# Kernel tuning notes

Measured on AMD Instinct MI355X. Metric: run time of the kernel, lower is better.

The kernel has to match this reference:

```python
import jax, jax.numpy as jnp
import numpy as np
from jax import lax

B, S, IN, H, C = 128, 128, 512, 256, 256  # batch, num_sentences, word_hidden*2, sentence_hidden, context
BN_EPS = 1e-5


def setup_inputs() -> dict:
    key = jax.random.key(0)
    ks = jax.random.split(key, 16)
    u = lambda k, shape: jax.random.uniform(k, shape, minval=-0.1, maxval=0.1, dtype=jnp.float32)
    return {
        "x": jax.random.normal(ks[0], (B, S, IN), jnp.float32),
        "sent_hidden_stat": jnp.zeros((2, B, H), jnp.float32),  # unused by forward (as in original)
        "num_sentences_lens": jax.random.randint(ks[1], (B,), 1, S + 1),
        # bidirectional GRU weights (PyTorch layout: [3H, in], gate order r,z,n)
        "w_ih_f": u(ks[2], (3 * H, IN)), "w_hh_f": u(ks[3], (3 * H, H)),
        "b_ih_f": u(ks[4], (3 * H,)),   "b_hh_f": u(ks[5], (3 * H,)),
        "w_ih_b": u(ks[6], (3 * H, IN)), "w_hh_b": u(ks[7], (3 * H, H)),
        "b_ih_b": u(ks[8], (3 * H,)),   "b_hh_b": u(ks[9], (3 * H,)),
        # sentence projection Linear(2H -> C)
        "proj_w": u(ks[10], (C, 2 * H)), "proj_b": u(ks[11], (C,)),
        # BatchNorm1d(num_features=S) affine params
        "bn_gamma": jnp.ones((S,), jnp.float32), "bn_beta": jnp.zeros((S,), jnp.float32),
        # sentence context vector [C, 1]
        "context": u(ks[12], (C, 1)),
    }


def _gru_dir(x, w_ih, w_hh, b_ih, b_hh):
    """Single-direction GRU over x: [B, T, IN] -> [B, T, H] (PyTorch GRU math)."""
    Hd = w_hh.shape[1]
    xp = jnp.einsum('bti,gi->tbg', x, w_ih) + b_ih  # [T, B, 3H], input projections precomputed

    def step(h, xpt):
        hp = h @ w_hh.T + b_hh
        xr, xz, xn = jnp.split(xpt, 3, axis=-1)
        hr, hz, hn = jnp.split(hp, 3, axis=-1)
        r = jax.nn.sigmoid(xr + hr)
        z = jax.nn.sigmoid(xz + hz)
        n = jnp.tanh(xn + r * hn)
        h_new = (1.0 - z) * n + z * h
        return h_new, h_new

    h0 = jnp.zeros((x.shape[0], Hd), x.dtype)
    _, ys = lax.scan(step, h0, xp)
    return jnp.swapaxes(ys, 0, 1)  # [B, T, H]


def reference(x, sent_hidden_stat, num_sentences_lens,
              w_ih_f, w_hh_f, b_ih_f, b_hh_f,
              w_ih_b, w_hh_b, b_ih_b, b_hh_b,
              proj_w, proj_b, bn_gamma, bn_beta, context):
    # Bidirectional GRU over sentences
    out_f = _gru_dir(x, w_ih_f, w_hh_f, b_ih_f, b_hh_f)
    out_b = _gru_dir(x[:, ::-1], w_ih_b, w_hh_b, b_ih_b, b_hh_b)[:, ::-1]
    out = jnp.concatenate([out_f, out_b], axis=-1)  # [B, S, 2H]

    # _fetch/get_mask: zero out positions beyond each document's sentence count
    mask = (jnp.arange(out.shape[1])[None, :] < num_sentences_lens[:, None]).astype(out.dtype)
    out = out * mask[:, :, None]

    # projection -> BatchNorm1d(num_features=S, training stats) -> ReLU
    proj = jnp.einsum('bsd,cd->bsc', out, proj_w) + proj_b  # [B, S, C]
    mu = proj.mean(axis=(0, 2), keepdims=True)
    var = jnp.mean((proj - mu) ** 2, axis=(0, 2), keepdims=True)
    bn = (proj - mu) / jnp.sqrt(var + BN_EPS) * bn_gamma[None, :, None] + bn_beta[None, :, None]
    p = jax.nn.relu(bn)

    # additive attention pooling over sentences
    scores = jnp.einsum('bsc,co->bs', p, context)  # [B, S]
    attn = jax.nn.softmax(scores, axis=1)
    return jnp.einsum('bs,bsd->bd', attn, out)  # [B, 2H]
```

## Files before the change

### kernel.cpp

```cpp
#include <hip/hip_runtime.h>
#include <hip/hip_bf16.h>

#define B_   128
#define S_   128
#define IN_  512
#define H_   256
#define G3_  768
#define C_   256
#define D2H_ 512

typedef short bf16x8 __attribute__((ext_vector_type(8)));
typedef float f32x4  __attribute__((ext_vector_type(4)));

static __device__ __forceinline__ short f2bf(float f) {
  unsigned u = __float_as_uint(f);
  return (short)((u + 0x7fffu + ((u >> 16) & 1u)) >> 16);
}
static __device__ __forceinline__ float bf2f(unsigned short v) {
  return __uint_as_float((unsigned)v << 16);
}

static __device__ __forceinline__ void async16(const void* g, const void* l) {
  __builtin_amdgcn_global_load_lds(
      (const __attribute__((address_space(1))) void*)g,
      (__attribute__((address_space(3))) void*)l, 16, 0, 0);
}

__global__ __launch_bounds__(1024) void pack_wh(
    const float* __restrict__ whf, const float* __restrict__ whb,
    unsigned short* __restrict__ wp)
{
  const int o = blockIdx.x * 1024 + threadIdx.x;
  const int j    = o & 7;
  const int lane = (o >> 3) & 63;
  const int kk   = (o >> 9) & 7;
  const int tt   = (o >> 12) & 1;
  const int rest = o >> 13;
  const int g    = rest % 3;
  const int wv   = (rest / 3) & 7;
  const int dir  = rest / 24;
  const float* w = dir ? whb : whf;
  const int row = wv * 32 + tt * 16 + (lane & 15);
  const int k   = kk * 32 + (lane >> 4) * 8 + j;
  wp[o] = (unsigned short)f2bf(w[(size_t)(g * H_ + row) * H_ + k]);
}

__global__ __launch_bounds__(256) void xp_gemm_bf(
    const float* __restrict__ x,
    const float* __restrict__ wf, const float* __restrict__ wb,
    const float* __restrict__ bif, const float* __restrict__ bhf,
    const float* __restrict__ bib, const float* __restrict__ bhb,
    unsigned short* __restrict__ xpf, unsigned short* __restrict__ xpb)
{
  const int sb = blockIdx.x;
  const int bn = blockIdx.y;
  const bool fwd = (bn < 6);
  const float* __restrict__ wsrc = fwd ? wf : wb;
  const float* __restrict__ bi   = fwd ? bif : bib;
  const float* __restrict__ bh   = fwd ? bhf : bhb;
  const int nloc0 = (fwd ? bn : bn - 6) * 128;

  __shared__ __align__(16) unsigned short As[128][56];
  __shared__ __align__(16) unsigned short Bs[128][56];

  const int tid  = threadIdx.x;
  const int wave = tid >> 6, lane = tid & 63;
  const int col  = lane & 15, lg = lane >> 4;
  const int wm   = wave >> 1, wn = wave & 1;
  const int rr   = tid >> 1;
  const int hf   = (tid & 1) * 16;

  const float* ax = x    + ((size_t)(rr * 128 + sb) * IN_ + hf);
  const float* bx = wsrc + ((size_t)(nloc0 + rr) * IN_ + hf);

  f32x4 acc[4][4];
#pragma unroll
  for (int i = 0; i < 4; ++i)
#pragma unroll
    for (int j = 0; j < 4; ++j) acc[i][j] = f32x4{0.f, 0.f, 0.f, 0.f};

  for (int k0 = 0; k0 < IN_; k0 += 32) {
    float4 a0 = *(const float4*)(ax + k0);
    float4 a1 = *(const float4*)(ax + k0 + 4);
    float4 a2 = *(const float4*)(ax + k0 + 8);
    float4 a3 = *(const float4*)(ax + k0 + 12);
    float4 c0 = *(const float4*)(bx + k0);
    float4 c1 = *(const float4*)(bx + k0 + 4);
    float4 c2 = *(const float4*)(bx + k0 + 8);
    float4 c3 = *(const float4*)(bx + k0 + 12);
    __syncthreads();
    {
      bf16x8 p0, p1;
      p0[0]=f2bf(a0.x); p0[1]=f2bf(a0.y); p0[2]=f2bf(a0.z); p0[3]=f2bf(a0.w);
      p0[4]=f2bf(a1.x); p0[5]=f2bf(a1.y); p0[6]=f2bf(a1.z); p0[7]=f2bf(a1.w);
      p1[0]=f2bf(a2.x); p1[1]=f2bf(a2.y); p1[2]=f2bf(a2.z); p1[3]=f2bf(a2.w);
      p1[4]=f2bf(a3.x); p1[5]=f2bf(a3.y); p1[6]=f2bf(a3.z); p1[7]=f2bf(a3.w);
      *(bf16x8*)&As[rr][hf]     = p0;
      *(bf16x8*)&As[rr][hf + 8] = p1;
      p0[0]=f2bf(c0.x); p0[1]=f2bf(c0.y); p0[2]=f2bf(c0.z); p0[3]=f2bf(c0.w);
      p0[4]=f2bf(c1.x); p0[5]=f2bf(c1.y); p0[6]=f2bf(c1.z); p0[7]=f2bf(c1.w);
      p1[0]=f2bf(c2.x); p1[1]=f2bf(c2.y); p1[2]=f2bf(c2.z); p1[3]=f2bf(c2.w);
      p1[4]=f2bf(c3.x); p1[5]=f2bf(c3.y); p1[6]=f2bf(c3.z); p1[7]=f2bf(c3.w);
      *(bf16x8*)&Bs[rr][hf]     = p0;
      *(bf16x8*)&Bs[rr][hf + 8] = p1;
    }
    __syncthreads();
    bf16x8 af[4], bfv[4];
#pragma unroll
    for (int mi = 0; mi < 4; ++mi)
      af[mi] = *(const bf16x8*)&As[wm * 64 + mi * 16 + col][lg * 8];
#pragma unroll
    for (int ni = 0; ni < 4; ++ni)
      bfv[ni] = *(const bf16x8*)&Bs[wn * 64 + ni * 16 + col][lg * 8];
#pragma unroll
    for (int mi = 0; mi < 4; ++mi)
#pragma unroll
      for (int ni = 0; ni < 4; ++ni)
        acc[mi][ni] = __builtin_amdgcn_mfma_f32_16x16x32_bf16(af[mi], bfv[ni], acc[mi][ni], 0, 0, 0);
  }

  const int t = fwd ? sb : (S_ - 1 - sb);
  unsigned short* __restrict__ dstbase = fwd ? xpf : xpb;
#pragma unroll
  for (int ni = 0; ni < 4; ++ni) {
    const int g = nloc0 + wn * 64 + ni * 16 + col;
    const float bias = bi[g] + (g < 2 * H_ ? bh[g] : 0.f);
#pragma unroll
    for (int mi = 0; mi < 4; ++mi) {
      const int grp = wm * 16 + mi * 4 + lg;
      ushort4 o;
      o.x = (unsigned short)f2bf(acc[mi][ni][0] + bias);
      o.y = (unsigned short)f2bf(acc[mi][ni][1] + bias);
      o.z = (unsigned short)f2bf(acc[mi][ni][2] + bias);
      o.w = (unsigned short)f2bf(acc[mi][ni][3] + bias);
      *(ushort4*)(dstbase + (((size_t)t * 32 + grp) * G3_ + g) * 4) = o;
    }
  }
}

__global__ __launch_bounds__(512, 2) void gru_mfma(
    const unsigned short* __restrict__ xpf, const unsigned short* __restrict__ xpb,
    const unsigned short* __restrict__ wp,
    const float* __restrict__ bhf, const float* __restrict__ bhb,
    const int* __restrict__ lens, float* __restrict__ out)
{
  const int dir  = blockIdx.x >> 5;
  const int grpb = blockIdx.x & 31;
  const int b0   = grpb * 4;
  const unsigned short* __restrict__ xp = dir ? xpb : xpf;
  const float* __restrict__ bhh = dir ? bhb : bhf;

  const int tid  = threadIdx.x;
  const int wave = tid >> 6;
  const int lane = tid & 63;
  const int col  = lane & 15;
  const int lg   = lane >> 4;
  const int gb0  = wave * 32 + col;

  __shared__ __align__(16) unsigned short hlds[2][32][16][8];
  __shared__ __align__(16) unsigned short xlds[2][G3_ * 4];

  ((int4*)hlds)[tid]       = int4{0, 0, 0, 0};
  ((int4*)hlds)[512 + tid] = int4{0, 0, 0, 0};

  {
    const unsigned short* base = xp + (size_t)grpb * (G3_ * 4);
    if (tid < 384)
      async16(base + (size_t)tid * 8, (const char*)&xlds[0][0] + wave * 1024);
  }

  const unsigned short* wpb = wp + (size_t)(dir * 8 + wave) * 24576 + lane * 8;

  bf16x8 wrz[2][2][8];
#pragma unroll
  for (int tt = 0; tt < 2; ++tt)
#pragma unroll
    for (int g = 0; g < 2; ++g)
#pragma unroll
      for (int kk = 0; kk < 8; ++kk)
        wrz[tt][g][kk] = *(const bf16x8*)(wpb + (((g * 2 + tt) * 8 + kk) << 9));

  float bhn[2];
  bhn[0] = bhh[2 * H_ + gb0];
  bhn[1] = bhh[2 * H_ + gb0 + 16];

  int len_[4];
#pragma unroll
  for (int i = 0; i < 4; ++i) len_[i] = lens[b0 + i];

  float hreg[2][4] = {};

  const int s0 = dir ? (S_ - 1) : 0;
  float* op[4];
#pragma unroll
  for (int i = 0; i < 4; ++i)
    op[i] = out + ((size_t)(b0 + i) * S_ + s0) * D2H_ + dir * H_ + gb0;
  const ptrdiff_t sdelta = dir ? -(ptrdiff_t)D2H_ : (ptrdiff_t)D2H_;

  int p = 0;
  for (int t = 0; t < S_; ++t) {
    __syncthreads();
    const int xb = t & 1;

    bf16x8 wn[2][8];
#pragma unroll
    for (int tt = 0; tt < 2; ++tt)
#pragma unroll
      for (int kk = 0; kk < 8; ++kk)
        wn[tt][kk] = *(const bf16x8*)(wpb + (((4 + tt) * 8 + kk) << 9));

    if (t > 0 && lg == 0) {
      const int s_prev = dir ? (S_ - t) : (t - 1);
#pragma unroll
      for (int i = 0; i < 4; ++i) {
        const bool m = s_prev < len_[i];
        op[i][0]  = m ? hreg[0][i] : 0.f;
        op[i][16] = m ? hreg[1][i] : 0.f;
        op[i] += sdelta;
      }
    }

    if (t + 1 < S_) {
      const unsigned short* base = xp + ((size_t)(t + 1) * 32 + grpb) * (G3_ * 4);
      if (tid < 384)
        async16(base + (size_t)tid * 8, (const char*)&xlds[xb ^ 1][0] + wave * 1024);
    }

#pragma unroll
    for (int tt = 0; tt < 2; ++tt) {
      const int u = gb0 + tt * 16;
      ushort4 r4 = *(const ushort4*)&xlds[xb][u * 4];
      ushort4 z4 = *(const ushort4*)&xlds[xb][(H_ + u) * 4];
      f32x4 accr, accz, accn;
      accr[0] = bf2f(r4.x); accr[1] = bf2f(r4.y); accr[2] = bf2f(r4.z); accr[3] = bf2f(r4.w);
      accz[0] = bf2f(z4.x); accz[1] = bf2f(z4.y); accz[2] = bf2f(z4.z); accz[3] = bf2f(z4.w);
      accn = f32x4{bhn[tt], bhn[tt], bhn[tt], bhn[tt]};
#pragma unroll
      for (int kk = 0; kk < 8; ++kk) {
        bf16x8 a = *(const bf16x8*)&hlds[p][kk * 4 + lg][col][0];
        accr = __builtin_amdgcn_mfma_f32_16x16x32_bf16(a, wrz[tt][0][kk], accr, 0, 0, 0);
        accz = __builtin_amdgcn_mfma_f32_16x16x32_bf16(a, wrz[tt][1][kk], accz, 0, 0, 0);
        accn = __builtin_amdgcn_mfma_f32_16x16x32_bf16(a, wn[tt][kk], accn, 0, 0, 0);
      }
      ushort4 n4 = *(const ushort4*)&xlds[xb][(2 * H_ + u) * 4];
      float hnv[4];
#pragma unroll
      for (int i = 0; i < 4; ++i) {
        float r  = 1.f / (1.f + __expf(-accr[i]));
        float z  = 1.f / (1.f + __expf(-accz[i]));
        float nx = bf2f((&n4.x)[i]) + r * accn[i];
        float n  = 1.f - 2.f / (__expf(2.f * nx) + 1.f);
        float hn = n + z * (hreg[tt][i] - n);
        hreg[tt][i] = hn;
        hnv[i] = hn;
      }
      if (lg == 0) {
        unsigned pk01, pk23;
        asm("v_cvt_pk_bf16_f32 %0, %1, %2" : "=v"(pk01) : "v"(hnv[0]), "v"(hnv[1]));
        asm("v_cvt_pk_bf16_f32 %0, %1, %2" : "=v"(pk23) : "v"(hnv[2]), "v"(hnv[3]));
        const int kb = u >> 3, jj = u & 7;
        hlds[p ^ 1][kb][0][jj] = (unsigned short)(pk01 & 0xffffu);
        hlds[p ^ 1][kb][1][jj] = (unsigned short)(pk01 >> 16);
        hlds[p ^ 1][kb][2][jj] = (unsigned short)(pk23 & 0xffffu);
        hlds[p ^ 1][kb][3][jj] = (unsigned short)(pk23 >> 16);
      }
    }
    p ^= 1;
  }

  if (lg == 0) {
    const int s_last = dir ? 0 : (S_ - 1);
#pragma unroll
    for (int i = 0; i < 4; ++i) {
      const bool m = s_last < len_[i];
      op[i][0]  = m ? hreg[0][i] : 0.f;
      op[i][16] = m ? hreg[1][i] : 0.f;
    }
  }
}

__global__ __launch_bounds__(256) void proj_gemm(
    const float* __restrict__ a, const float* __restrict__ w,
    const float* __restrict__ bias, float* __restrict__ proj)
{
  const int bm = blockIdx.x;
  const int n0 = blockIdx.y * 64;

  __shared__ float As[16][68];
  __shared__ float Bs[16][68];

  const int tid = threadIdx.x;
  const int row = tid >> 2;
  const int kq  = (tid & 3) << 2;
  const int tx  = tid & 15, ty = tid >> 4;

  const float* arow = a + (size_t)(bm * 64 + row) * D2H_ + kq;
  const float* brow = w + (size_t)(n0 + row) * D2H_ + kq;

  float acc[4][4] = {};

  for (int k0 = 0; k0 < D2H_; k0 += 16) {
    float4 av = *(const float4*)(arow + k0);
    float4 bv = *(const float4*)(brow + k0);
    As[kq + 0][row] = av.x; As[kq + 1][row] = av.y;
    As[kq + 2][row] = av.z; As[kq + 3][row] = av.w;
    Bs[kq + 0][row] = bv.x; Bs[kq + 1][row] = bv.y;
    Bs[kq + 2][row] = bv.z; Bs[kq + 3][row] = bv.w;
    __syncthreads();
#pragma unroll
    for (int k = 0; k < 16; ++k) {
      float4 av2 = *(const float4*)&As[k][ty * 4];
      float4 bv2 = *(const float4*)&Bs[k][tx * 4];
      acc[0][0] += av2.x * bv2.x; acc[0][1] += av2.x * bv2.y; acc[0][2] += av2.x * bv2.z; acc[0][3] += av2.x * bv2.w;
      acc[1][0] += av2.y * bv2.x; acc[1][1] += av2.y * bv2.y; acc[1][2] += av2.y * bv2.z; acc[1][3] += av2.y * bv2.w;
      acc[2][0] += av2.z * bv2.x; acc[2][1] += av2.z * bv2.y; acc[2][2] += av2.z * bv2.z; acc[2][3] += av2.z * bv2.w;
      acc[3][0] += av2.w * bv2.x; acc[3][1] += av2.w * bv2.y; acc[3][2] += av2.w * bv2.z; acc[3][3] += av2.w * bv2.w;
    }
    __syncthreads();
  }

  float4 bv4 = *(const float4*)(bias + n0 + tx * 4);
#pragma unroll
  for (int i = 0; i < 4; ++i) {
    int m = bm * 64 + ty * 4 + i;
    float4 o;
    o.x = acc[i][0] + bv4.x; o.y = acc[i][1] + bv4.y;
    o.z = acc[i][2] + bv4.z; o.w = acc[i][3] + bv4.w;
    *(float4*)(proj + (size_t)m * C_ + n0 + tx * 4) = o;
  }
}

__global__ __launch_bounds__(256) void bn_stats(
    const float* __restrict__ proj, float* __restrict__ mu, float* __restrict__ rstd)
{
  const int s = blockIdx.x, tid = threadIdx.x;
  float sum = 0.f, sq = 0.f;
  for (int b = 0; b < B_; ++b) {
    float v = proj[((size_t)b * S_ + s) * C_ + tid];
    sum += v; sq += v * v;
  }
#pragma unroll
  for (int o = 32; o; o >>= 1) { sum += __shfl_down(sum, o); sq += __shfl_down(sq, o); }
  __shared__ float r1[4], r2[4];
  const int lane = tid & 63, wid = tid >> 6;
  if (!lane) { r1[wid] = sum; r2[wid] = sq; }
  __syncthreads();
  if (!tid) {
    float s1 = r1[0] + r1[1] + r1[2] + r1[3];
    float s2 = r2[0] + r2[1] + r2[2] + r2[3];
    float m = s1 / (float)(B_ * C_);
    float var = s2 / (float)(B_ * C_) - m * m;
    mu[s] = m;
    rstd[s] = rsqrtf(var + 1e-5f);
  }
}

__global__ __launch_bounds__(256) void score_k(
    const float* __restrict__ proj, const float* __restrict__ mu,
    const float* __restrict__ rstd, const float* __restrict__ gamma,
    const float* __restrict__ beta, const float* __restrict__ ctx,
    float* __restrict__ scores)
{
  const int wid = threadIdx.x >> 6, lane = threadIdx.x & 63;
  const int m = blockIdx.x * 4 + wid;
  const int s = m & 127;
  float4 v  = *(const float4*)(proj + (size_t)m * C_ + lane * 4);
  float4 cv = *(const float4*)(ctx + lane * 4);
  const float ms = mu[s], rs = rstd[s], g = gamma[s], be = beta[s];
  float acc = fmaxf((v.x - ms) * rs * g + be, 0.f) * cv.x
            + fmaxf((v.y - ms) * rs * g + be, 0.f) * cv.y
            + fmaxf((v.z - ms) * rs * g + be, 0.f) * cv.z
            + fmaxf((v.w - ms) * rs * g + be, 0.f) * cv.w;
#pragma unroll
  for (int o = 32; o; o >>= 1) acc += __shfl_down(acc, o);
  if (!lane) scores[m] = acc;
}

__global__ __launch_bounds__(128) void softmax_k(
    const float* __restrict__ scores, float* __restrict__ attn)
{
  const int b = blockIdx.x, tid = threadIdx.x;
  float v = scores[b * S_ + tid];
  float mx = v;
#pragma unroll
  for (int o = 32; o; o >>= 1) mx = fmaxf(mx, __shfl_down(mx, o));
  __shared__ float t0[2], t1[2];
  const int lane = tid & 63, wid = tid >> 6;
  if (!lane) t0[wid] = mx;
  __syncthreads();
  mx = fmaxf(t0[0], t0[1]);
  float e = __expf(v - mx);
  float ssum = e;
#pragma unroll
  for (int o = 32; o; o >>= 1) ssum += __shfl_down(ssum, o);
  if (!lane) t1[wid] = ssum;
  __syncthreads();
  attn[b * S_ + tid] = e / (t1[0] + t1[1]);
}

__global__ __launch_bounds__(512) void final_k(
    const float* __restrict__ attn, const float* __restrict__ out,
    float* __restrict__ y)
{
  const int b = blockIdx.x, d = threadIdx.x;
  __shared__ float a[S_];
  if (threadIdx.x < S_) a[threadIdx.x] = attn[b * S_ + threadIdx.x];
  __syncthreads();
  float acc = 0.f;
  for (int s = 0; s < S_; ++s)
    acc += a[s] * out[((size_t)b * S_ + s) * D2H_ + d];
  y[(size_t)b * D2H_ + d] = acc;
}

extern "C" void kernel_launch(void* const* d_in, const int* in_sizes, int n_in,
                              void* d_out, int out_size, void* d_ws, size_t ws_size,
                              hipStream_t stream)
{
  const float* x      = (const float*)d_in[0];
  const int*   lens   = (const int*)d_in[2];
  const float* w_ih_f = (const float*)d_in[3];
  const float* w_hh_f = (const float*)d_in[4];
  const float* b_ih_f = (const float*)d_in[5];
  const float* b_hh_f = (const float*)d_in[6];
  const float* w_ih_b = (const float*)d_in[7];
  const float* w_hh_b = (const float*)d_in[8];
  const float* b_ih_b = (const float*)d_in[9];
  const float* b_hh_b = (const float*)d_in[10];
  const float* proj_w = (const float*)d_in[11];
  const float* proj_b = (const float*)d_in[12];
  const float* gamma  = (const float*)d_in[13];
  const float* beta   = (const float*)d_in[14];
  const float* ctx    = (const float*)d_in[15];

  float* ws = (float*)d_ws;
  float* outm = ws;
  unsigned short* xpf = (unsigned short*)(ws + 8388608);
  unsigned short* xpb = xpf + 12582912;
  unsigned short* wp  = xpb + 12582912;
  float* proj   = ws + 8388608;
  float* mu     = ws + 12582912;
  float* rstd   = ws + 12583040;
  float* scores = ws + 12583168;
  float* attn   = ws + 12599552;

  pack_wh<<<384, 1024, 0, stream>>>(w_hh_f, w_hh_b, wp);
  xp_gemm_bf<<<dim3(128, 12), 256, 0, stream>>>(
      x, w_ih_f, w_ih_b, b_ih_f, b_hh_f, b_ih_b, b_hh_b, xpf, xpb);
  gru_mfma<<<64, 512, 0, stream>>>(xpf, xpb, wp, b_hh_f, b_hh_b, lens, outm);
  proj_gemm<<<dim3(256, 4), 256, 0, stream>>>(outm, proj_w, proj_b, proj);
  bn_stats<<<128, 256, 0, stream>>>(proj, mu, rstd);
  score_k<<<4096, 256, 0, stream>>>(proj, mu, rstd, gamma, beta, ctx, scores);
  softmax_k<<<128, 128, 0, stream>>>(scores, attn);
  final_k<<<128, 512, 0, stream>>>(attn, outm, (float*)d_out);
}
```

Baseline: 460.8 us.

## Pin GRU recurrent r/z weights in AGPRs and stage n-gate weights in LDS

```diff
diff --git a/kernel.cpp b/kernel.cpp
--- a/kernel.cpp
+++ b/kernel.cpp
@@ -25,6 +25,54 @@
       (const __attribute__((address_space(1))) void*)g,
       (__attribute__((address_space(3))) void*)l, 16, 0, 0);
 }
+
+#define AGPR_CLOB \
+  "a0","a1","a2","a3","a4","a5","a6","a7","a8","a9",\
+  "a10","a11","a12","a13","a14","a15","a16","a17","a18","a19",\
+  "a20","a21","a22","a23","a24","a25","a26","a27","a28","a29",\
+  "a30","a31","a32","a33","a34","a35","a36","a37","a38","a39",\
+  "a40","a41","a42","a43","a44","a45","a46","a47","a48","a49",\
+  "a50","a51","a52","a53","a54","a55","a56","a57","a58","a59",\
+  "a60","a61","a62","a63","a64","a65","a66","a67","a68","a69",\
+  "a70","a71","a72","a73","a74","a75","a76","a77","a78","a79",\
+  "a80","a81","a82","a83","a84","a85","a86","a87","a88","a89",\
+  "a90","a91","a92","a93","a94","a95","a96","a97","a98","a99",\
+  "a100","a101","a102","a103","a104","a105","a106","a107","a108","a109",\
+  "a110","a111","a112","a113","a114","a115","a116","a117","a118","a119",\
+  "a120","a121","a122","a123","a124","a125","a126","a127","a128","a129",\
+  "a130","a131","a132","a133","a134","a135","a136","a137","a138","a139",\
+  "a140","a141","a142","a143","a144","a145","a146","a147","a148","a149",\
+  "a150","a151","a152","a153","a154","a155","a156","a157","a158","a159",\
+  "a160","a161","a162","a163","a164","a165","a166","a167","a168","a169",\
+  "a170","a171","a172","a173","a174","a175","a176","a177","a178","a179",\
+  "a180","a181","a182","a183","a184","a185","a186","a187","a188","a189",\
+  "a190","a191","a192","a193","a194","a195","a196","a197","a198","a199",\
+  "a200","a201","a202","a203","a204","a205","a206","a207","a208","a209",\
+  "a210","a211","a212","a213","a214","a215","a216","a217","a218","a219",\
+  "a220","a221","a222","a223","a224","a225","a226","a227","a228","a229",\
+  "a230","a231","a232","a233","a234","a235","a236","a237","a238","a239",\
+  "a240","a241","a242","a243","a244","a245","a246","a247","a248","a249",\
+  "a250","a251","a252","a253","a254","a255"
+
+#define PINFRAG(off, A0, A1, A2, A3) do {                                   \
+  int4 q_;                                                                  \
+  asm volatile("global_load_dwordx4 %0, %1, off\n\ts_waitcnt vmcnt(0)"      \
+               : "=v"(q_) : "v"(wpb + (off)));                              \
+  asm volatile("v_accvgpr_write_b32 " A0 ", %0\n\t"                         \
+               "v_accvgpr_write_b32 " A1 ", %1\n\t"                         \
+               "v_accvgpr_write_b32 " A2 ", %2\n\t"                         \
+               "v_accvgpr_write_b32 " A3 ", %3"                             \
+               :: "v"(q_.x), "v"(q_.y), "v"(q_.z), "v"(q_.w)                \
+               : A0, A1, A2, A3);                                           \
+} while (0)
+
+#define MFMA1(acc, af, AB)                                                  \
+  asm volatile("v_mfma_f32_16x16x32_bf16 %0, %1, " AB ", %0"                \
+               : "+v"(acc) : "v"(af) : AGPR_CLOB)
+
+#define MFMA1V(acc, af, bf)                                                 \
+  asm volatile("v_mfma_f32_16x16x32_bf16 %0, %1, %2, %0"                    \
+               : "+v"(acc) : "v"(af), "v"(bf) : AGPR_CLOB)
 
 __global__ __launch_bounds__(1024) void pack_wh(
     const float* __restrict__ whf, const float* __restrict__ whb,
@@ -138,7 +186,7 @@
   }
 }
 
-__global__ __launch_bounds__(512, 2) void gru_mfma(
+__global__ __launch_bounds__(256) void gru_mfma(
     const unsigned short* __restrict__ xpf, const unsigned short* __restrict__ xpb,
     const unsigned short* __restrict__ wp,
     const float* __restrict__ bhf, const float* __restrict__ bhb,
@@ -155,60 +203,145 @@
   const int lane = tid & 63;
   const int col  = lane & 15;
   const int lg   = lane >> 4;
-  const int gb0  = wave * 32 + col;
+  const int ub   = wave * 64 + col;
 
   __shared__ __align__(16) unsigned short hlds[2][32][16][8];
   __shared__ __align__(16) unsigned short xlds[2][G3_ * 4];
-
-  ((int4*)hlds)[tid]       = int4{0, 0, 0, 0};
-  ((int4*)hlds)[512 + tid] = int4{0, 0, 0, 0};
+  __shared__ __align__(16) unsigned short nlds[65536];
+
+#pragma unroll
+  for (int k = 0; k < 4; ++k)
+    ((int4*)hlds)[k * 256 + tid] = int4{0, 0, 0, 0};
+
+  const unsigned short* wpb = wp + (size_t)(dir * 8 + 2 * wave) * 24576 + lane * 8;
+  PINFRAG(0,     "a0","a1","a2","a3");     PINFRAG(512,   "a4","a5","a6","a7");
+  PINFRAG(1024,  "a8","a9","a10","a11");   PINFRAG(1536,  "a12","a13","a14","a15");
+  PINFRAG(2048,  "a16","a17","a18","a19"); PINFRAG(2560,  "a20","a21","a22","a23");
+  PINFRAG(3072,  "a24","a25","a26","a27"); PINFRAG(3584,  "a28","a29","a30","a31");
+  PINFRAG(4096,  "a32","a33","a34","a35"); PINFRAG(4608,  "a36","a37","a38","a39");
+  PINFRAG(5120,  "a40","a41","a42","a43"); PINFRAG(5632,  "a44","a45","a46","a47");
+  PINFRAG(6144,  "a48","a49","a50","a51"); PINFRAG(6656,  "a52","a53","a54","a55");
+  PINFRAG(7168,  "a56","a57","a58","a59"); PINFRAG(7680,  "a60","a61","a62","a63");
+  PINFRAG(24576, "a64","a65","a66","a67"); PINFRAG(25088, "a68","a69","a70","a71");
+  PINFRAG(25600, "a72","a73","a74","a75"); PINFRAG(26112, "a76","a77","a78","a79");
+  PINFRAG(26624, "a80","a81","a82","a83"); PINFRAG(27136, "a84","a85","a86","a87");
+  PINFRAG(27648, "a88","a89","a90","a91"); PINFRAG(28160, "a92","a93","a94","a95");
+  PINFRAG(28672, "a96","a97","a98","a99");    PINFRAG(29184, "a100","a101","a102","a103");
+  PINFRAG(29696, "a104","a105","a106","a107");PINFRAG(30208, "a108","a109","a110","a111");
+  PINFRAG(30720, "a112","a113","a114","a115");PINFRAG(31232, "a116","a117","a118","a119");
+  PINFRAG(31744, "a120","a121","a122","a123");PINFRAG(32256, "a124","a125","a126","a127");
+  PINFRAG(8192,  "a128","a129","a130","a131");PINFRAG(8704,  "a132","a133","a134","a135");
+  PINFRAG(9216,  "a136","a137","a138","a139");PINFRAG(9728,  "a140","a141","a142","a143");
+  PINFRAG(10240, "a144","a145","a146","a147");PINFRAG(10752, "a148","a149","a150","a151");
+  PINFRAG(11264, "a152","a153","a154","a155");PINFRAG(11776, "a156","a157","a158","a159");
+  PINFRAG(12288, "a160","a161","a162","a163");PINFRAG(12800, "a164","a165","a166","a167");
+  PINFRAG(13312, "a168","a169","a170","a171");PINFRAG(13824, "a172","a173","a174","a175");
+  PINFRAG(14336, "a176","a177","a178","a179");PINFRAG(14848, "a180","a181","a182","a183");
+  PINFRAG(15360, "a184","a185","a186","a187");PINFRAG(15872, "a188","a189","a190","a191");
+  PINFRAG(32768, "a192","a193","a194","a195");PINFRAG(33280, "a196","a197","a198","a199");
+  PINFRAG(33792, "a200","a201","a202","a203");PINFRAG(34304, "a204","a205","a206","a207");
+  PINFRAG(34816, "a208","a209","a210","a211");PINFRAG(35328, "a212","a213","a214","a215");
+  PINFRAG(35840, "a216","a217","a218","a219");PINFRAG(36352, "a220","a221","a222","a223");
+  PINFRAG(36864, "a224","a225","a226","a227");PINFRAG(37376, "a228","a229","a230","a231");
+  PINFRAG(37888, "a232","a233","a234","a235");PINFRAG(38400, "a236","a237","a238","a239");
+  PINFRAG(38912, "a240","a241","a242","a243");PINFRAG(39424, "a244","a245","a246","a247");
+  PINFRAG(39936, "a248","a249","a250","a251");PINFRAG(40448, "a252","a253","a254","a255");
+
+  for (int j = 0; j < 32; ++j) {
+    const int c  = j * 4 + wave;
+    const int wt = c >> 5, tq = (c >> 3) & 3, kk = c & 7;
+    const unsigned short* src = wp
+        + (size_t)(dir * 8 + wt * 2 + (tq >> 1)) * 24576
+        + 16384 + (tq & 1) * 4096 + kk * 512 + lane * 8;
+    async16(src, (const char*)&nlds[0] + (size_t)c * 1024);
+  }
 
   {
     const unsigned short* base = xp + (size_t)grpb * (G3_ * 4);
-    if (tid < 384)
-      async16(base + (size_t)tid * 8, (const char*)&xlds[0][0] + wave * 1024);
-  }
-
-  const unsigned short* wpb = wp + (size_t)(dir * 8 + wave) * 24576 + lane * 8;
-
-  bf16x8 wrz[2][2][8];
-#pragma unroll
-  for (int tt = 0; tt < 2; ++tt)
-#pragma unroll
-    for (int g = 0; g < 2; ++g)
-#pragma unroll
-      for (int kk = 0; kk < 8; ++kk)
-        wrz[tt][g][kk] = *(const bf16x8*)(wpb + (((g * 2 + tt) * 8 + kk) << 9));
-
-  float bhn[2];
-  bhn[0] = bhh[2 * H_ + gb0];
-  bhn[1] = bhh[2 * H_ + gb0 + 16];
+#pragma unroll
+    for (int j = 0; j < 2; ++j) {
+      const int c = j * 256 + tid;
+      if (c < 384)
+        async16(base + (size_t)c * 8,
+                (const char*)&xlds[0][0] + (size_t)(j * 256 + wave * 64) * 16);
+    }
+  }
+
+  float bhn[4];
+#pragma unroll
+  for (int tq = 0; tq < 4; ++tq) bhn[tq] = bhh[2 * H_ + ub + tq * 16];
 
   int len_[4];
 #pragma unroll
   for (int i = 0; i < 4; ++i) len_[i] = lens[b0 + i];
 
-  float hreg[2][4] = {};
+  float hreg[4][4] = {};
 
   const int s0 = dir ? (S_ - 1) : 0;
   float* op[4];
 #pragma unroll
   for (int i = 0; i < 4; ++i)
-    op[i] = out + ((size_t)(b0 + i) * S_ + s0) * D2H_ + dir * H_ + gb0;
+    op[i] = out + ((size_t)(b0 + i) * S_ + s0) * D2H_ + dir * H_ + ub;
   const ptrdiff_t sdelta = dir ? -(ptrdiff_t)D2H_ : (ptrdiff_t)D2H_;
+
+#define TQ_BODY(TQc, R0,R1,R2,R3,R4,R5,R6,R7, Z0,Z1,Z2,Z3,Z4,Z5,Z6,Z7)       \
+  {                                                                           \
+    const int u = ub + (TQc) * 16;                                            \
+    const unsigned short* nb = &nlds[((wave * 4 + (TQc)) << 12) + lane * 8];  \
+    bf16x8 nf0 = *(const bf16x8*)(nb);                                        \
+    bf16x8 nf1 = *(const bf16x8*)(nb + 512);                                  \
+    bf16x8 nf2 = *(const bf16x8*)(nb + 1024);                                 \
+    bf16x8 nf3 = *(const bf16x8*)(nb + 1536);                                 \
+    bf16x8 nf4 = *(const bf16x8*)(nb + 2048);                                 \
+    bf16x8 nf5 = *(const bf16x8*)(nb + 2560);                                 \
+    bf16x8 nf6 = *(const bf16x8*)(nb + 3072);                                 \
+    bf16x8 nf7 = *(const bf16x8*)(nb + 3584);                                 \
+    ushort4 r4 = *(const ushort4*)&xlds[xb][u * 4];                           \
+    ushort4 z4 = *(const ushort4*)&xlds[xb][(H_ + u) * 4];                    \
+    f32x4 accr, accz, accn;                                                   \
+    accr[0]=bf2f(r4.x); accr[1]=bf2f(r4.y); accr[2]=bf2f(r4.z); accr[3]=bf2f(r4.w); \
+    accz[0]=bf2f(z4.x); accz[1]=bf2f(z4.y); accz[2]=bf2f(z4.z); accz[3]=bf2f(z4.w); \
+    accn = f32x4{bhn[TQc], bhn[TQc], bhn[TQc], bhn[TQc]};                     \
+    asm volatile("s_nop 3" : "+v"(accr), "+v"(accz), "+v"(accn));             \
+    MFMA1(accr, afr[0], R0); MFMA1(accz, afr[0], Z0); MFMA1V(accn, afr[0], nf0); \
+    MFMA1(accr, afr[1], R1); MFMA1(accz, afr[1], Z1); MFMA1V(accn, afr[1], nf1); \
+    MFMA1(accr, afr[2], R2); MFMA1(accz, afr[2], Z2); MFMA1V(accn, afr[2], nf2); \
+    MFMA1(accr, afr[3], R3); MFMA1(accz, afr[3], Z3); MFMA1V(accn, afr[3], nf3); \
+    MFMA1(accr, afr[4], R4); MFMA1(accz, afr[4], Z4); MFMA1V(accn, afr[4], nf4); \
+    MFMA1(accr, afr[5], R5); MFMA1(accz, afr[5], Z5); MFMA1V(accn, afr[5], nf5); \
+    MFMA1(accr, afr[6], R6); MFMA1(accz, afr[6], Z6); MFMA1V(accn, afr[6], nf6); \
+    MFMA1(accr, afr[7], R7); MFMA1(accz, afr[7], Z7); MFMA1V(accn, afr[7], nf7); \
+    asm volatile("s_nop 7\n\ts_nop 7\n\ts_nop 7"                              \
+                 : "+v"(accr), "+v"(accz), "+v"(accn));                       \
+    ushort4 n4 = *(const ushort4*)&xlds[xb][(2 * H_ + u) * 4];                \
+    float hnv[4];                                                             \
+    _Pragma("unroll")                                                         \
+    for (int i = 0; i < 4; ++i) {                                             \
+      float r  = 1.f / (1.f + __expf(-accr[i]));                              \
+      float z  = 1.f / (1.f + __expf(-accz[i]));                              \
+      float nx = bf2f((&n4.x)[i]) + r * accn[i];                              \
+      float n  = 1.f - 2.f / (__expf(2.f * nx) + 1.f);                        \
+      float hn = n + z * (hreg[TQc][i] - n);                                  \
+      hreg[TQc][i] = hn;                                                      \
+      hnv[i] = hn;                                                            \
+    }                                                                         \
+    if (lg == 0) {                                                            \
+      unsigned pk01, pk23;                                                    \
+      asm("v_cvt_pk_bf16_f32 %0, %1, %2" : "=v"(pk01) : "v"(hnv[0]), "v"(hnv[1])); \
+      asm("v_cvt_pk_bf16_f32 %0, %1, %2" : "=v"(pk23) : "v"(hnv[2]), "v"(hnv[3])); \
+      const int kb = u >> 3, jj = u & 7;                                      \
+      hlds[p ^ 1][kb][0][jj] = (unsigned short)(pk01 & 0xffffu);              \
+      hlds[p ^ 1][kb][1][jj] = (unsigned short)(pk01 >> 16);                  \
+      hlds[p ^ 1][kb][2][jj] = (unsigned short)(pk23 & 0xffffu);              \
+      hlds[p ^ 1][kb][3][jj] = (unsigned short)(pk23 >> 16);                  \
+    }                                                                         \
+  }
 
   int p = 0;
   for (int t = 0; t < S_; ++t) {
     __syncthreads();
     const int xb = t & 1;
 
-    bf16x8 wn[2][8];
-#pragma unroll
-    for (int tt = 0; tt < 2; ++tt)
-#pragma unroll
-      for (int kk = 0; kk < 8; ++kk)
-        wn[tt][kk] = *(const bf16x8*)(wpb + (((4 + tt) * 8 + kk) << 9));
-
     if (t > 0 && lg == 0) {
       const int s_prev = dir ? (S_ - t) : (t - 1);
 #pragma unroll
@@ -216,57 +349,40 @@
         const bool m = s_prev < len_[i];
         op[i][0]  = m ? hreg[0][i] : 0.f;
         op[i][16] = m ? hreg[1][i] : 0.f;
+        op[i][32] = m ? hreg[2][i] : 0.f;
+        op[i][48] = m ? hreg[3][i] : 0.f;
         op[i] += sdelta;
       }
     }
 
     if (t + 1 < S_) {
       const unsigned short* base = xp + ((size_t)(t + 1) * 32 + grpb) * (G3_ * 4);
-      if (tid < 384)
-        async16(base + (size_t)tid * 8, (const char*)&xlds[xb ^ 1][0] + wave * 1024);
-    }
-
-#pragma unroll
-    for (int tt = 0; tt < 2; ++tt) {
-      const int u = gb0 + tt * 16;
-      ushort4 r4 = *(const ushort4*)&xlds[xb][u * 4];
-      ushort4 z4 = *(const ushort4*)&xlds[xb][(H_ + u) * 4];
-      f32x4 accr, accz, accn;
-      accr[0] = bf2f(r4.x); accr[1] = bf2f(r4.y); accr[2] = bf2f(r4.z); accr[3] = bf2f(r4.w);
-      accz[0] = bf2f(z4.x); accz[1] = bf2f(z4.y); accz[2] = bf2f(z4.z); accz[3] = bf2f(z4.w);
-      accn = f32x4{bhn[tt], bhn[tt], bhn[tt], bhn[tt]};
-#pragma unroll
-      for (int kk = 0; kk < 8; ++kk) {
-        bf16x8 a = *(const bf16x8*)&hlds[p][kk * 4 + lg][col][0];
-        accr = __builtin_amdgcn_mfma_f32_16x16x32_bf16(a, wrz[tt][0][kk], accr, 0, 0, 0);
-        accz = __builtin_amdgcn_mfma_f32_16x16x32_bf16(a, wrz[tt][1][kk], accz, 0, 0, 0);
-        accn = __builtin_amdgcn_mfma_f32_16x16x32_bf16(a, wn[tt][kk], accn, 0, 0, 0);
+#pragma unroll
+      for (int j = 0; j < 2; ++j) {
+        const int c = j * 256 + tid;
+        if (c < 384)
+          async16(base + (size_t)c * 8,
+                  (const char*)&xlds[xb ^ 1][0] + (size_t)(j * 256 + wave * 64) * 16);
       }
-      ushort4 n4 = *(const ushort4*)&xlds[xb][(2 * H_ + u) * 4];
-      float hnv[4];
-#pragma unroll
-      for (int i = 0; i < 4; ++i) {
-        float r  = 1.f / (1.f + __expf(-accr[i]));
-        float z  = 1.f / (1.f + __expf(-accz[i]));
-        float nx = bf2f((&n4.x)[i]) + r * accn[i];
-        float n  = 1.f - 2.f / (__expf(2.f * nx) + 1.f);
-        float hn = n + z * (hreg[tt][i] - n);
-        hreg[tt][i] = hn;
-        hnv[i] = hn;
-      }
-      if (lg == 0) {
-        unsigned pk01, pk23;
-        asm("v_cvt_pk_bf16_f32 %0, %1, %2" : "=v"(pk01) : "v"(hnv[0]), "v"(hnv[1]));
-        asm("v_cvt_pk_bf16_f32 %0, %1, %2" : "=v"(pk23) : "v"(hnv[2]), "v"(hnv[3]));
-        const int kb = u >> 3, jj = u & 7;
-        hlds[p ^ 1][kb][0][jj] = (unsigned short)(pk01 & 0xffffu);
-        hlds[p ^ 1][kb][1][jj] = (unsigned short)(pk01 >> 16);
-        hlds[p ^ 1][kb][2][jj] = (unsigned short)(pk23 & 0xffffu);
-        hlds[p ^ 1][kb][3][jj] = (unsigned short)(pk23 >> 16);
-      }
-    }
+    }
+
+    bf16x8 afr[8];
+#pragma unroll
+    for (int kk = 0; kk < 8; ++kk)
+      afr[kk] = *(const bf16x8*)&hlds[p][kk * 4 + lg][col][0];
+
+    TQ_BODY(0, "a[0:3]","a[4:7]","a[8:11]","a[12:15]","a[16:19]","a[20:23]","a[24:27]","a[28:31]",
+               "a[128:131]","a[132:135]","a[136:139]","a[140:143]","a[144:147]","a[148:151]","a[152:155]","a[156:159]")
+    TQ_BODY(1, "a[32:35]","a[36:39]","a[40:43]","a[44:47]","a[48:51]","a[52:55]","a[56:59]","a[60:63]",
+               "a[160:163]","a[164:167]","a[168:171]","a[172:175]","a[176:179]","a[180:183]","a[184:187]","a[188:191]")
+    TQ_BODY(2, "a[64:67]","a[68:71]","a[72:75]","a[76:79]","a[80:83]","a[84:87]","a[88:91]","a[92:95]",
+               "a[192:195]","a[196:199]","a[200:203]","a[204:207]","a[208:211]","a[212:215]","a[216:219]","a[220:223]")
+    TQ_BODY(3, "a[96:99]","a[100:103]","a[104:107]","a[108:111]","a[112:115]","a[116:119]","a[120:123]","a[124:127]",
+               "a[224:227]","a[228:231]","a[232:235]","a[236:239]","a[240:243]","a[244:247]","a[248:251]","a[252:255]")
+
     p ^= 1;
   }
+#undef TQ_BODY
 
   if (lg == 0) {
     const int s_last = dir ? 0 : (S_ - 1);
@@ -275,6 +391,8 @@
       const bool m = s_last < len_[i];
       op[i][0]  = m ? hreg[0][i] : 0.f;
       op[i][16] = m ? hreg[1][i] : 0.f;
+      op[i][32] = m ? hreg[2][i] : 0.f;
+      op[i][48] = m ? hreg[3][i] : 0.f;
     }
   }
 }
@@ -446,7 +564,7 @@
   pack_wh<<<384, 1024, 0, stream>>>(w_hh_f, w_hh_b, wp);
   xp_gemm_bf<<<dim3(128, 12), 256, 0, stream>>>(
       x, w_ih_f, w_ih_b, b_ih_f, b_hh_f, b_ih_b, b_hh_b, xpf, xpb);
-  gru_mfma<<<64, 512, 0, stream>>>(xpf, xpb, wp, b_hh_f, b_hh_b, lens, outm);
+  gru_mfma<<<64, 256, 0, stream>>>(xpf, xpb, wp, b_hh_f, b_hh_b, lens, outm);
   proj_gemm<<<dim3(256, 4), 256, 0, stream>>>(outm, proj_w, proj_b, proj);
   bn_stats<<<128, 256, 0, stream>>>(proj, mu, rstd);
   score_k<<<4096, 256, 0, stream>>>(proj, mu, rstd, gamma, beta, ctx, scores);
```

Result: slower. 568.6 us (+23.4%).
